# Kernel optimization log

Hardware: AMD Instinct MI355X
Metric: run time of the kernel (lower is better)

Reference implementation:

```python
import jax, jax.numpy as jnp
import numpy as np

N_HEADS = 16
HEAD = 64
SEQ = 2048
EMBED = 1024
BATCH = 4

def setup_inputs() -> dict:
    key = jax.random.key(0)
    ks = jax.random.split(key, 6)
    inputs = jax.random.normal(ks[0], (BATCH, SEQ, EMBED), dtype=jnp.float32)
    # per-head projection weights stacked: [H, E, D] (nn.Linear(E, D, bias=False))
    s = 1.0 / np.sqrt(EMBED)
    Wq = jax.random.uniform(ks[1], (N_HEADS, EMBED, HEAD), jnp.float32, -s, s)
    Wk = jax.random.uniform(ks[2], (N_HEADS, EMBED, HEAD), jnp.float32, -s, s)
    Wv = jax.random.uniform(ks[3], (N_HEADS, EMBED, HEAD), jnp.float32, -s, s)
    Wo = jax.random.uniform(ks[4], (EMBED, EMBED), jnp.float32, -s, s)
    bo = jax.random.uniform(ks[5], (EMBED,), jnp.float32, -s, s)
    return {"inputs": inputs, "Wq": Wq, "Wk": Wk, "Wv": Wv, "Wo": Wo, "bo": bo}

def reference(inputs, Wq, Wk, Wv, Wo, bo):
    B, S, E = inputs.shape
    # batched per-head projections: [B,S,E] x [H,E,D] -> [B,H,S,D]
    q = jnp.einsum('bse,hed->bhsd', inputs, Wq)
    k = jnp.einsum('bse,hed->bhsd', inputs, Wk)
    v = jnp.einsum('bse,hed->bhsd', inputs, Wv)
    q = q / jnp.sqrt(jnp.float32(HEAD)).astype(q.dtype)
    scores = jnp.einsum('bhsd,bhtd->bhst', q, k)  # [B,H,S,S]
    causal = jnp.tril(jnp.ones((S, S), dtype=bool))
    scores = jnp.where(causal, scores, jnp.finfo(scores.dtype).min)
    weights = jax.nn.softmax(scores, axis=-1)
    out = jnp.einsum('bhst,bhtd->bhsd', weights, v)  # [B,H,S,D]
    # concat heads in head order -> [B,S,H*D]
    out = jnp.transpose(out, (0, 2, 1, 3)).reshape(B, S, N_HEADS * HEAD)
    return out @ Wo.T + bo
```

## Files before the change

### kernel.cpp

```cpp
#include <hip/hip_runtime.h>
#include <stdint.h>

typedef unsigned short ushort_t;
typedef __attribute__((ext_vector_type(8))) short short8;
typedef __attribute__((ext_vector_type(4))) short bf16x4;
typedef __attribute__((ext_vector_type(4))) float f32x4;

#define AS1 __attribute__((address_space(1)))
#define AS3 __attribute__((address_space(3)))

__device__ __forceinline__ void gl_lds16(const void* g, void* l) {
    __builtin_amdgcn_global_load_lds((const AS1 unsigned int*)g,
                                     (AS3 unsigned int*)l, 16, 0, 0);
}

__device__ __forceinline__ ushort_t f2bf(float f) {
    union { float f; unsigned u; } v; v.f = f;
    unsigned r = v.u + 0x7fffu + ((v.u >> 16) & 1u);
    return (ushort_t)(r >> 16);
}

__global__ __launch_bounds__(256) void prep_k(const float* __restrict__ inp,
                                              const float* __restrict__ Wo,
                                              const float* __restrict__ Wq,
                                              const float* __restrict__ Wk,
                                              const float* __restrict__ Wv,
                                              ushort_t* __restrict__ inp_bf,
                                              ushort_t* __restrict__ WoB,
                                              ushort_t* __restrict__ WT) {
    const int bx = blockIdx.x, tid = threadIdx.x;
    if (bx < 4608) {
        const float* src = (bx < 4096) ? inp : Wo;
        ushort_t* dst    = (bx < 4096) ? inp_bf : WoB;
        int i = ((bx < 4096 ? bx : bx - 4096) * 256 + tid) * 8;
        float4 a = *(const float4*)(src + i);
        float4 b = *(const float4*)(src + i + 4);
        short8 o;
        o[0] = (short)f2bf(a.x); o[1] = (short)f2bf(a.y);
        o[2] = (short)f2bf(a.z); o[3] = (short)f2bf(a.w);
        o[4] = (short)f2bf(b.x); o[5] = (short)f2bf(b.y);
        o[6] = (short)f2bf(b.z); o[7] = (short)f2bf(b.w);
        *(short8*)(dst + i) = o;
        return;
    }
    __shared__ ushort_t t[64 * 65];
    const int wb = bx - 4608;
    const int mat = wb >> 8;
    const int h   = (wb >> 4) & 15;
    const int et  = wb & 15;
    const float* W = (mat == 0 ? Wq : (mat == 1 ? Wk : Wv)) + h * (1024 * 64);
    const float* src = W + et * 64 * 64;
#pragma unroll
    for (int i = 0; i < 16; ++i) {
        int idx = i * 256 + tid;
        int e = idx >> 6, d = idx & 63;
        t[e * 65 + d] = f2bf(src[idx]);
    }
    __syncthreads();
    ushort_t* dst = WT + (mat * 16 + h) * (64 * 1024) + et * 64;
#pragma unroll
    for (int i = 0; i < 16; ++i) {
        int idx = i * 256 + tid;
        int d = idx >> 6, e = idx & 63;
        dst[d * 1024 + e] = t[e * 65 + d];
    }
}

__global__ __launch_bounds__(512, 2) void qkv_k(const ushort_t* __restrict__ A,
                                                const ushort_t* __restrict__ WT,
                                                ushort_t* __restrict__ Q,
                                                ushort_t* __restrict__ K,
                                                ushort_t* __restrict__ Vt) {
    __shared__ __align__(16) ushort_t ring[49152];
    const int tid = threadIdx.x, wave = tid >> 6, lane = tid & 63;
    const int ln15 = lane & 15, quad = lane >> 4;
    const int wm = wave >> 1, wn = wave & 1;
    const int flat = blockIdx.y * 32 + blockIdx.x;
    const int nfb  = (flat & 7) * 96 + (flat >> 3);
    const int m0 = (nfb & 31) * 256, n0 = (nfb >> 5) * 128;

    const int sa_row = wave * 16 + (lane >> 2);
    const int sa_col = (lane & 3) * 8;
    const int woff   = wave * 512;

    f32x4 acc[4][4];
#pragma unroll
    for (int i = 0; i < 4; ++i)
#pragma unroll
        for (int j = 0; j < 4; ++j)
#pragma unroll
            for (int e = 0; e < 4; ++e) acc[i][j][e] = 0.f;

    auto stage = [&](int t) {
        const int kb = t * 32;
        ushort_t* buf = &ring[(t & 3) * 12288];
        gl_lds16(A  + (size_t)(m0 + sa_row)       * 1024 + kb + sa_col, buf + woff);
        gl_lds16(A  + (size_t)(m0 + 128 + sa_row) * 1024 + kb + sa_col, buf + 4096 + woff);
        gl_lds16(WT + (size_t)(n0 + sa_row)       * 1024 + kb + sa_col, buf + 8192 + woff);
    };

    stage(0); stage(1); stage(2);
    asm volatile("s_waitcnt vmcnt(6)" ::: "memory");
    __builtin_amdgcn_s_barrier();
    __builtin_amdgcn_sched_barrier(0);

    for (int t = 0; t < 32; ++t) {
        const ushort_t* buf = &ring[(t & 3) * 12288];
        short8 a[4], b[4];
#pragma unroll
        for (int f = 0; f < 4; ++f)
            a[f] = *(const short8*)&buf[(wm * 64 + f * 16 + ln15) * 32 + quad * 8];
#pragma unroll
        for (int f = 0; f < 4; ++f)
            b[f] = *(const short8*)&buf[8192 + (wn * 64 + f * 16 + ln15) * 32 + quad * 8];
        if (t + 3 < 32) stage(t + 3);
        if (t < 29)       asm volatile("s_waitcnt vmcnt(6)" ::: "memory");
        else if (t == 29) asm volatile("s_waitcnt vmcnt(3)" ::: "memory");
        else if (t == 30) asm volatile("s_waitcnt vmcnt(0)" ::: "memory");
        __builtin_amdgcn_s_setprio(1);
#pragma unroll
        for (int fm = 0; fm < 4; ++fm)
#pragma unroll
            for (int fn = 0; fn < 4; ++fn)
                acc[fm][fn] = __builtin_amdgcn_mfma_f32_16x16x32_bf16(a[fm], b[fn], acc[fm][fn], 0, 0, 0);
        __builtin_amdgcn_s_setprio(0);
        __builtin_amdgcn_s_barrier();
        __builtin_amdgcn_sched_barrier(0);
    }

    const int n_base = n0 + wn * 64;
    const int mat = n_base >> 10;
    const int h   = (n_base >> 6) & 15;
    if (mat < 2) {
        ushort_t* dst = (mat == 0) ? Q : K;
        const float scale = (mat == 0) ? 0.125f : 1.0f;
#pragma unroll
        for (int fm = 0; fm < 4; ++fm) {
#pragma unroll
            for (int r = 0; r < 4; ++r) {
                int mg = m0 + wm * 64 + fm * 16 + quad * 4 + r;
                int bi = mg >> 11, s = mg & 2047;
                size_t base = ((size_t)(bi * 16 + h) * 2048 + s) * 64;
#pragma unroll
                for (int fn = 0; fn < 4; ++fn)
                    dst[base + fn * 16 + ln15] = f2bf(acc[fm][fn][r] * scale);
            }
        }
    } else {
        ushort_t* tb = &ring[wave * 6144];
#pragma unroll
        for (int fn = 0; fn < 4; ++fn)
#pragma unroll
            for (int fm = 0; fm < 4; ++fm) {
                bf16x4 pk;
#pragma unroll
                for (int r = 0; r < 4; ++r) pk[r] = (short)f2bf(acc[fm][fn][r]);
                *(bf16x4*)&tb[(fn * 16 + ln15) * 72 + fm * 16 + quad * 4] = pk;
            }
        const int s0 = m0 + wm * 64;
        const int bi = s0 >> 11, sb = s0 & 2047;
#pragma unroll
        for (int p = 0; p < 8; ++p) {
            int d  = p * 8 + (lane >> 3);
            int sc = (lane & 7) * 8;
            short8 vv = *(const short8*)&tb[d * 72 + sc];
            *(short8*)&Vt[((size_t)(bi * 16 + h) * 64 + d) * 2048 + sb + sc] = vv;
        }
    }
}

__global__ __launch_bounds__(256, 3) void flash_k(const ushort_t* Q, const ushort_t* K,
                                                  const ushort_t* Vt, ushort_t* Aout) {
    __shared__ __align__(16) ushort_t Ks[2][64 * 64];
    __shared__ __align__(16) ushort_t Vts[2][64 * 64];
    __shared__ __align__(16) ushort_t PT[4][32 * 72];
    const int tid = threadIdx.x, wave = tid >> 6, lane = tid & 63;
    const int ln15 = lane & 15, quad = lane >> 4;
    const int bx = blockIdx.x;
    const int qt = 15 - (bx >> 6);
    const int bh = bx & 63;
    const int qw = qt * 128 + wave * 32;
    const ushort_t* Kb = K + (size_t)bh * 2048 * 64;
    const ushort_t* Vb = Vt + (size_t)bh * 64 * 2048;
    ushort_t* myPT = PT[wave];
    const int srow = tid >> 3, c8 = (tid & 7) * 8;

    short8 qf[2][2];
    {
        const ushort_t* Qb = Q + (size_t)bh * 2048 * 64;
#pragma unroll
        for (int qs = 0; qs < 2; ++qs)
#pragma unroll
            for (int kk = 0; kk < 2; ++kk)
                qf[qs][kk] = *(const short8*)&Qb[(size_t)(qw + qs * 16 + ln15) * 64 + kk * 32 + quad * 8];
    }

    f32x4 o[4][2];
#pragma unroll
    for (int dt = 0; dt < 4; ++dt)
#pragma unroll
        for (int qs = 0; qs < 2; ++qs)
#pragma unroll
            for (int e = 0; e < 4; ++e) o[dt][qs][e] = 0.f;
    float l_s[2] = {0.f, 0.f};

    const int ktEnd = 2 * qt + 2;
    gl_lds16(Kb + (size_t)srow * 64 + c8,        &Ks[0][srow * 64 + c8]);
    gl_lds16(Kb + (size_t)(32 + srow) * 64 + c8, &Ks[0][(32 + srow) * 64 + c8]);
    gl_lds16(Vb + (size_t)srow * 2048 + c8,        &Vts[0][srow * 64 + c8]);
    gl_lds16(Vb + (size_t)(32 + srow) * 2048 + c8, &Vts[0][(32 + srow) * 64 + c8]);
    __syncthreads();

    for (int kt = 0; kt < ktEnd; ++kt) {
        const int cur = kt & 1, nxt = cur ^ 1;
        if (kt + 1 < ktEnd) {
            int kn = kt + 1;
            gl_lds16(Kb + (size_t)(kn * 64 + srow) * 64 + c8,      &Ks[nxt][srow * 64 + c8]);
            gl_lds16(Kb + (size_t)(kn * 64 + 32 + srow) * 64 + c8, &Ks[nxt][(32 + srow) * 64 + c8]);
            gl_lds16(Vb + (size_t)srow * 2048 + kn * 64 + c8,        &Vts[nxt][srow * 64 + c8]);
            gl_lds16(Vb + (size_t)(32 + srow) * 2048 + kn * 64 + c8, &Vts[nxt][(32 + srow) * 64 + c8]);
        }
        if (kt * 64 <= qw + 31) {
            f32x4 sc[4][2];
#pragma unroll
            for (int ks = 0; ks < 4; ++ks) {
#pragma unroll
                for (int qs = 0; qs < 2; ++qs)
#pragma unroll
                    for (int e = 0; e < 4; ++e) sc[ks][qs][e] = 0.f;
#pragma unroll
                for (int kk = 0; kk < 2; ++kk) {
                    short8 kf = *(const short8*)&Ks[cur][(ks * 16 + ln15) * 64 + kk * 32 + quad * 8];
#pragma unroll
                    for (int qs = 0; qs < 2; ++qs)
                        sc[ks][qs] = __builtin_amdgcn_mfma_f32_16x16x32_bf16(kf, qf[qs][kk], sc[ks][qs], 0, 0, 0);
                }
            }
            if (kt * 64 + 63 > qw) {
#pragma unroll
                for (int ks = 0; ks < 4; ++ks)
#pragma unroll
                    for (int qs = 0; qs < 2; ++qs) {
                        int qg = qw + qs * 16 + ln15;
#pragma unroll
                        for (int r = 0; r < 4; ++r) {
                            int kg = kt * 64 + ks * 16 + quad * 4 + r;
                            if (kg > qg) sc[ks][qs][r] = -1e30f;
                        }
                    }
            }
#pragma unroll
            for (int qs = 0; qs < 2; ++qs) {
#pragma unroll
                for (int ks = 0; ks < 4; ++ks) {
                    bf16x4 pk;
#pragma unroll
                    for (int r = 0; r < 4; ++r) {
                        float p = __expf(sc[ks][qs][r]);
                        l_s[qs] += p;
                        pk[r] = (short)f2bf(p);
                    }
                    *(bf16x4*)&myPT[(qs * 16 + ln15) * 72 + ks * 16 + quad * 4] = pk;
                }
            }
            short8 pf[2][2];
#pragma unroll
            for (int qs = 0; qs < 2; ++qs)
#pragma unroll
                for (int kk = 0; kk < 2; ++kk)
                    pf[qs][kk] = *(const short8*)&myPT[(qs * 16 + ln15) * 72 + kk * 32 + quad * 8];
#pragma unroll
            for (int dt = 0; dt < 4; ++dt)
#pragma unroll
                for (int kk = 0; kk < 2; ++kk) {
                    short8 vf = *(const short8*)&Vts[cur][(dt * 16 + ln15) * 64 + kk * 32 + quad * 8];
#pragma unroll
                    for (int qs = 0; qs < 2; ++qs)
                        o[dt][qs] = __builtin_amdgcn_mfma_f32_16x16x32_bf16(vf, pf[qs][kk], o[dt][qs], 0, 0, 0);
                }
        }
        __syncthreads();
    }
#pragma unroll
    for (int qs = 0; qs < 2; ++qs) {
        float l = l_s[qs];
        l += __shfl_xor(l, 16);
        l += __shfl_xor(l, 32);
        float inv = 1.f / l;
#pragma unroll
        for (int dt = 0; dt < 4; ++dt) {
            bf16x4 pk;
#pragma unroll
            for (int r = 0; r < 4; ++r) pk[r] = (short)f2bf(o[dt][qs][r] * inv);
            *(bf16x4*)&myPT[(qs * 16 + ln15) * 72 + dt * 16 + quad * 4] = pk;
        }
    }
    const int bi = bh >> 4, h = bh & 15;
#pragma unroll
    for (int p = 0; p < 4; ++p) {
        int row = p * 8 + (lane >> 3);
        int cc = (lane & 7) * 8;
        short8 vv = *(const short8*)&myPT[row * 72 + cc];
        int qg = qw + row;
        *(short8*)&Aout[((size_t)bi * 2048 + qg) * 1024 + h * 64 + cc] = vv;
    }
}

__global__ __launch_bounds__(256) void outproj_k(const ushort_t* A, const ushort_t* WoB,
                                                 const float* bo, float* Out) {
    __shared__ __align__(16) ushort_t As[2][128 * 64];
    __shared__ __align__(16) ushort_t Bs[2][128 * 64];
    const int tid = threadIdx.x, wave = tid >> 6, lane = tid & 63;
    const int ln15 = lane & 15, quad = lane >> 4;
    const int wm = wave >> 1, wn = wave & 1;
    const int lrow = lane >> 3, lcol = (lane & 7) * 8;
    const int m0 = blockIdx.x * 128, n0 = blockIdx.y * 128;

    f32x4 acc[4][4];
#pragma unroll
    for (int i = 0; i < 4; ++i)
#pragma unroll
        for (int j = 0; j < 4; ++j)
#pragma unroll
            for (int e = 0; e < 4; ++e) acc[i][j][e] = 0.f;

#pragma unroll
    for (int i = 0; i < 4; ++i) {
        int br = i * 32 + wave * 8;
        gl_lds16(A   + (size_t)(m0 + br + lrow) * 1024 + lcol, &As[0][br * 64]);
        gl_lds16(WoB + (size_t)(n0 + br + lrow) * 1024 + lcol, &Bs[0][br * 64]);
    }
    __syncthreads();

    for (int it = 0; it < 16; ++it) {
        const int cur = it & 1, nxt = cur ^ 1;
        if (it < 15) {
            const int k0 = (it + 1) * 64;
#pragma unroll
            for (int i = 0; i < 4; ++i) {
                int br = i * 32 + wave * 8;
                gl_lds16(A   + (size_t)(m0 + br + lrow) * 1024 + k0 + lcol, &As[nxt][br * 64]);
                gl_lds16(WoB + (size_t)(n0 + br + lrow) * 1024 + k0 + lcol, &Bs[nxt][br * 64]);
            }
        }
#pragma unroll
        for (int kk = 0; kk < 2; ++kk) {
            short8 a[4], b[4];
#pragma unroll
            for (int f = 0; f < 4; ++f)
                a[f] = *(const short8*)&As[cur][(wm * 64 + f * 16 + ln15) * 64 + kk * 32 + quad * 8];
#pragma unroll
            for (int f = 0; f < 4; ++f)
                b[f] = *(const short8*)&Bs[cur][(wn * 64 + f * 16 + ln15) * 64 + kk * 32 + quad * 8];
#pragma unroll
            for (int fm = 0; fm < 4; ++fm)
#pragma unroll
                for (int fn = 0; fn < 4; ++fn)
                    acc[fm][fn] = __builtin_amdgcn_mfma_f32_16x16x32_bf16(a[fm], b[fn], acc[fm][fn], 0, 0, 0);
        }
        __syncthreads();
    }
#pragma unroll
    for (int fn = 0; fn < 4; ++fn) {
        int n = n0 + wn * 64 + fn * 16 + ln15;
        float bias = bo[n];
#pragma unroll
        for (int fm = 0; fm < 4; ++fm)
#pragma unroll
            for (int r = 0; r < 4; ++r) {
                int mg = m0 + wm * 64 + fm * 16 + quad * 4 + r;
                Out[(size_t)mg * 1024 + n] = acc[fm][fn][r] + bias;
            }
    }
}

extern "C" void kernel_launch(void* const* d_in, const int* in_sizes, int n_in,
                              void* d_out, int out_size, void* d_ws, size_t ws_size,
                              hipStream_t stream) {
    (void)in_sizes; (void)n_in; (void)out_size; (void)ws_size;
    const float* inp = (const float*)d_in[0];
    const float* Wq  = (const float*)d_in[1];
    const float* Wk  = (const float*)d_in[2];
    const float* Wv  = (const float*)d_in[3];
    const float* Wo  = (const float*)d_in[4];
    const float* bo  = (const float*)d_in[5];
    float* out = (float*)d_out;

    ushort_t* ws = (ushort_t*)d_ws;
    ushort_t* R0  = ws;
    ushort_t* WT  = R0  + 8388608;
    ushort_t* WoB = WT  + 3145728;
    ushort_t* Qb  = WoB + 1048576;
    ushort_t* Kb  = Qb  + 8388608;
    ushort_t* Vtb = Kb  + 8388608;

    ushort_t* inp_bf = R0;
    ushort_t* At     = R0;

    prep_k<<<5376, 256, 0, stream>>>(inp, Wo, Wq, Wk, Wv, inp_bf, WoB, WT);
    qkv_k<<<dim3(32, 24), 512, 0, stream>>>(inp_bf, WT, Qb, Kb, Vtb);
    flash_k<<<dim3(1024), 256, 0, stream>>>(Qb, Kb, Vtb, At);
    outproj_k<<<dim3(64, 8), 256, 0, stream>>>(At, WoB, bo, out);
}
```

Measured before the change: 264.9 us.

## XOR-swizzle LDS tiles in qkv, flash and outproj kernels; drop block remap

Applies an XOR swizzle to the 16-byte chunk positions of tiles staged through global_load_lds in three kernels. The global source column is permuted while the LDS destination stays linear, and the matching MFMA fragment reads use the same XOR, so row-strided short8 reads hit different LDS banks. The aim is to remove bank conflicts on fragment loads. The qkv kernel also drops its L2-friendly block-index remapping in favour of plain blockIdx tiling, which may lower cache locality.

```diff
diff --git a/kernel.cpp b/kernel.cpp
--- a/kernel.cpp
+++ b/kernel.cpp
@@ -75,13 +75,12 @@
     const int tid = threadIdx.x, wave = tid >> 6, lane = tid & 63;
     const int ln15 = lane & 15, quad = lane >> 4;
     const int wm = wave >> 1, wn = wave & 1;
-    const int flat = blockIdx.y * 32 + blockIdx.x;
-    const int nfb  = (flat & 7) * 96 + (flat >> 3);
-    const int m0 = (nfb & 31) * 256, n0 = (nfb >> 5) * 128;
-
-    const int sa_row = wave * 16 + (lane >> 2);
-    const int sa_col = (lane & 3) * 8;
-    const int woff   = wave * 512;
+    const int m0 = blockIdx.x * 256, n0 = blockIdx.y * 128;
+
+    const int sa_row  = wave * 16 + (lane >> 2);
+    const int sa_colS = (((lane & 3) ^ ((lane >> 3) & 3))) * 8;
+    const int woff    = wave * 512;
+    const int rchunk  = (quad ^ ((ln15 >> 1) & 3)) * 8;
 
     f32x4 acc[4][4];
 #pragma unroll
@@ -94,9 +93,9 @@
     auto stage = [&](int t) {
         const int kb = t * 32;
         ushort_t* buf = &ring[(t & 3) * 12288];
-        gl_lds16(A  + (size_t)(m0 + sa_row)       * 1024 + kb + sa_col, buf + woff);
-        gl_lds16(A  + (size_t)(m0 + 128 + sa_row) * 1024 + kb + sa_col, buf + 4096 + woff);
-        gl_lds16(WT + (size_t)(n0 + sa_row)       * 1024 + kb + sa_col, buf + 8192 + woff);
+        gl_lds16(A  + (size_t)(m0 + sa_row)       * 1024 + kb + sa_colS, buf + woff);
+        gl_lds16(A  + (size_t)(m0 + 128 + sa_row) * 1024 + kb + sa_colS, buf + 4096 + woff);
+        gl_lds16(WT + (size_t)(n0 + sa_row)       * 1024 + kb + sa_colS, buf + 8192 + woff);
     };
 
     stage(0); stage(1); stage(2);
@@ -109,10 +108,10 @@
         short8 a[4], b[4];
 #pragma unroll
         for (int f = 0; f < 4; ++f)
-            a[f] = *(const short8*)&buf[(wm * 64 + f * 16 + ln15) * 32 + quad * 8];
+            a[f] = *(const short8*)&buf[(wm * 64 + f * 16 + ln15) * 32 + rchunk];
 #pragma unroll
         for (int f = 0; f < 4; ++f)
-            b[f] = *(const short8*)&buf[8192 + (wn * 64 + f * 16 + ln15) * 32 + quad * 8];
+            b[f] = *(const short8*)&buf[8192 + (wn * 64 + f * 16 + ln15) * 32 + rchunk];
         if (t + 3 < 32) stage(t + 3);
         if (t < 29)       asm volatile("s_waitcnt vmcnt(6)" ::: "memory");
         else if (t == 29) asm volatile("s_waitcnt vmcnt(3)" ::: "memory");
@@ -184,6 +183,8 @@
     const ushort_t* Vb = Vt + (size_t)bh * 64 * 2048;
     ushort_t* myPT = PT[wave];
     const int srow = tid >> 3, c8 = (tid & 7) * 8;
+    const int c8s  = ((tid & 7) ^ ((tid >> 3) & 7)) * 8;
+    const int swr  = ln15 & 7;
 
     short8 qf[2][2];
     {
@@ -205,20 +206,20 @@
     float l_s[2] = {0.f, 0.f};
 
     const int ktEnd = 2 * qt + 2;
-    gl_lds16(Kb + (size_t)srow * 64 + c8,        &Ks[0][srow * 64 + c8]);
-    gl_lds16(Kb + (size_t)(32 + srow) * 64 + c8, &Ks[0][(32 + srow) * 64 + c8]);
-    gl_lds16(Vb + (size_t)srow * 2048 + c8,        &Vts[0][srow * 64 + c8]);
-    gl_lds16(Vb + (size_t)(32 + srow) * 2048 + c8, &Vts[0][(32 + srow) * 64 + c8]);
+    gl_lds16(Kb + (size_t)srow * 64 + c8s,        &Ks[0][srow * 64 + c8]);
+    gl_lds16(Kb + (size_t)(32 + srow) * 64 + c8s, &Ks[0][(32 + srow) * 64 + c8]);
+    gl_lds16(Vb + (size_t)srow * 2048 + c8s,        &Vts[0][srow * 64 + c8]);
+    gl_lds16(Vb + (size_t)(32 + srow) * 2048 + c8s, &Vts[0][(32 + srow) * 64 + c8]);
     __syncthreads();
 
     for (int kt = 0; kt < ktEnd; ++kt) {
         const int cur = kt & 1, nxt = cur ^ 1;
         if (kt + 1 < ktEnd) {
             int kn = kt + 1;
-            gl_lds16(Kb + (size_t)(kn * 64 + srow) * 64 + c8,      &Ks[nxt][srow * 64 + c8]);
-            gl_lds16(Kb + (size_t)(kn * 64 + 32 + srow) * 64 + c8, &Ks[nxt][(32 + srow) * 64 + c8]);
-            gl_lds16(Vb + (size_t)srow * 2048 + kn * 64 + c8,        &Vts[nxt][srow * 64 + c8]);
-            gl_lds16(Vb + (size_t)(32 + srow) * 2048 + kn * 64 + c8, &Vts[nxt][(32 + srow) * 64 + c8]);
+            gl_lds16(Kb + (size_t)(kn * 64 + srow) * 64 + c8s,      &Ks[nxt][srow * 64 + c8]);
+            gl_lds16(Kb + (size_t)(kn * 64 + 32 + srow) * 64 + c8s, &Ks[nxt][(32 + srow) * 64 + c8]);
+            gl_lds16(Vb + (size_t)srow * 2048 + kn * 64 + c8s,        &Vts[nxt][srow * 64 + c8]);
+            gl_lds16(Vb + (size_t)(32 + srow) * 2048 + kn * 64 + c8s, &Vts[nxt][(32 + srow) * 64 + c8]);
         }
         if (kt * 64 <= qw + 31) {
             f32x4 sc[4][2];
@@ -230,7 +231,7 @@
                     for (int e = 0; e < 4; ++e) sc[ks][qs][e] = 0.f;
 #pragma unroll
                 for (int kk = 0; kk < 2; ++kk) {
-                    short8 kf = *(const short8*)&Ks[cur][(ks * 16 + ln15) * 64 + kk * 32 + quad * 8];
+                    short8 kf = *(const short8*)&Ks[cur][(ks * 16 + ln15) * 64 + ((kk * 4 + quad) ^ swr) * 8];
 #pragma unroll
                     for (int qs = 0; qs < 2; ++qs)
                         sc[ks][qs] = __builtin_amdgcn_mfma_f32_16x16x32_bf16(kf, qf[qs][kk], sc[ks][qs], 0, 0, 0);
@@ -273,7 +274,7 @@
             for (int dt = 0; dt < 4; ++dt)
 #pragma unroll
                 for (int kk = 0; kk < 2; ++kk) {
-                    short8 vf = *(const short8*)&Vts[cur][(dt * 16 + ln15) * 64 + kk * 32 + quad * 8];
+                    short8 vf = *(const short8*)&Vts[cur][(dt * 16 + ln15) * 64 + ((kk * 4 + quad) ^ swr) * 8];
 #pragma unroll
                     for (int qs = 0; qs < 2; ++qs)
                         o[dt][qs] = __builtin_amdgcn_mfma_f32_16x16x32_bf16(vf, pf[qs][kk], o[dt][qs], 0, 0, 0);
@@ -314,6 +315,8 @@
     const int ln15 = lane & 15, quad = lane >> 4;
     const int wm = wave >> 1, wn = wave & 1;
     const int lrow = lane >> 3, lcol = (lane & 7) * 8;
+    const int lcolS = ((lane & 7) ^ (lane >> 3)) * 8;
+    const int swr   = ln15 & 7;
     const int m0 = blockIdx.x * 128, n0 = blockIdx.y * 128;
 
     f32x4 acc[4][4];
@@ -327,8 +330,8 @@
 #pragma unroll
     for (int i = 0; i < 4; ++i) {
         int br = i * 32 + wave * 8;
-        gl_lds16(A   + (size_t)(m0 + br + lrow) * 1024 + lcol, &As[0][br * 64]);
-        gl_lds16(WoB + (size_t)(n0 + br + lrow) * 1024 + lcol, &Bs[0][br * 64]);
+        gl_lds16(A   + (size_t)(m0 + br + lrow) * 1024 + lcolS, &As[0][br * 64]);
+        gl_lds16(WoB + (size_t)(n0 + br + lrow) * 1024 + lcolS, &Bs[0][br * 64]);
     }
     __syncthreads();
 
@@ -339,8 +342,8 @@
 #pragma unroll
             for (int i = 0; i < 4; ++i) {
                 int br = i * 32 + wave * 8;
-                gl_lds16(A   + (size_t)(m0 + br + lrow) * 1024 + k0 + lcol, &As[nxt][br * 64]);
-                gl_lds16(WoB + (size_t)(n0 + br + lrow) * 1024 + k0 + lcol, &Bs[nxt][br * 64]);
+                gl_lds16(A   + (size_t)(m0 + br + lrow) * 1024 + k0 + lcolS, &As[nxt][br * 64]);
+                gl_lds16(WoB + (size_t)(n0 + br + lrow) * 1024 + k0 + lcolS, &Bs[nxt][br * 64]);
             }
         }
 #pragma unroll
@@ -348,10 +351,10 @@
             short8 a[4], b[4];
 #pragma unroll
             for (int f = 0; f < 4; ++f)
-                a[f] = *(const short8*)&As[cur][(wm * 64 + f * 16 + ln15) * 64 + kk * 32 + quad * 8];
+                a[f] = *(const short8*)&As[cur][(wm * 64 + f * 16 + ln15) * 64 + ((kk * 4 + quad) ^ swr) * 8];
 #pragma unroll
             for (int f = 0; f < 4; ++f)
-                b[f] = *(const short8*)&Bs[cur][(wn * 64 + f * 16 + ln15) * 64 + kk * 32 + quad * 8];
+                b[f] = *(const short8*)&Bs[cur][(wn * 64 + f * 16 + ln15) * 64 + ((kk * 4 + quad) ^ swr) * 8];
 #pragma unroll
             for (int fm = 0; fm < 4; ++fm)
 #pragma unroll
```

Measured after the change: 234.7 us. 1.13x faster.
